# Optimization experiments

Hardware: AMD Instinct MI355X
Metric: run time of the kernel (lower is better)

The kernel has to match this reference:

```python
import jax, jax.numpy as jnp
import numpy as np

NUM_HEADS = 8
BN_EPS = 1e-5


def setup_inputs() -> dict:
    key = jax.random.key(0)
    ks = jax.random.split(key, 8)
    B, Ct, Cs, H, W, E = 8, 256, 128, 32, 32, 256
    s = 0.05  # small init scale to keep softmax logits reasonable
    return {
        "tgt": jax.random.normal(ks[0], (B, Ct, H, W), jnp.float32),
        "src": jax.random.normal(ks[1], (B, Cs, H, W), jnp.float32),
        "kv_w": jax.random.normal(ks[2], (E, Cs), jnp.float32) * s,
        "in_proj_w": jax.random.normal(ks[3], (3 * E, E), jnp.float32) * s,
        "in_proj_b": jnp.zeros((3 * E,), jnp.float32),
        "out_proj_w": jax.random.normal(ks[4], (E, E), jnp.float32) * s,
        "out_proj_b": jnp.zeros((E,), jnp.float32),
        "fuse_w": jax.random.normal(ks[5], (Ct, E), jnp.float32) * s,
        "bn_gamma": jnp.ones((Ct,), jnp.float32),
        "bn_beta": jnp.zeros((Ct,), jnp.float32),
        "bn_mean": jnp.zeros((Ct,), jnp.float32),
        "bn_var": jnp.ones((Ct,), jnp.float32),
    }


def reference(tgt, src, kv_w, in_proj_w, in_proj_b, out_proj_w, out_proj_b,
              fuse_w, bn_gamma, bn_beta, bn_mean, bn_var):
    B, Ct, H, W = tgt.shape
    E = kv_w.shape[0]
    nH = NUM_HEADS
    hd = E // nH

    # q_proj is Identity (C_tgt == embed_dim); flatten spatial to tokens [B, Q, E]
    q_seq = tgt.reshape(B, Ct, H * W).transpose(0, 2, 1)
    # kv_proj: 1x1 conv == channel matmul; then flatten to [B, K, E]
    kv_map = jnp.einsum('bchw,ec->behw', src, kv_w)
    k_seq = kv_map.reshape(B, E, H * W).transpose(0, 2, 1)

    # nn.MultiheadAttention: packed in-projection
    Wq, Wk, Wv = in_proj_w[:E], in_proj_w[E:2 * E], in_proj_w[2 * E:]
    bq, bk, bv = in_proj_b[:E], in_proj_b[E:2 * E], in_proj_b[2 * E:]
    qp = (q_seq @ Wq.T + bq).reshape(B, -1, nH, hd).transpose(0, 2, 1, 3)  # [B,h,Q,d]
    kp = (k_seq @ Wk.T + bk).reshape(B, -1, nH, hd).transpose(0, 2, 1, 3)  # [B,h,K,d]
    vp = (k_seq @ Wv.T + bv).reshape(B, -1, nH, hd).transpose(0, 2, 1, 3)  # [B,h,K,d]

    scores = jnp.einsum('bhqd,bhkd->bhqk', qp, kp) / jnp.sqrt(jnp.float32(hd))
    attn = jax.nn.softmax(scores, axis=-1)  # [B,h,Q,K] (non-flash explicit path)

    ctx = jnp.einsum('bhqk,bhkd->bhqd', attn, vp)
    ctx = ctx.transpose(0, 2, 1, 3).reshape(B, -1, E)  # [B,Q,E]
    out_seq = ctx @ out_proj_w.T + out_proj_b

    # cached spatial key-attention map: mean over heads and queries -> [B,1,Hk,Wk]
    attn_map = attn.mean(axis=(1, 2)).reshape(B, 1, H, W)

    # back to map, fuse: 1x1 conv -> BN(eval) -> SiLU, then residual add
    out_map = out_seq.transpose(0, 2, 1).reshape(B, E, H, W)
    fused = jnp.einsum('behw,ce->bchw', out_map, fuse_w)
    inv = bn_gamma / jnp.sqrt(bn_var + BN_EPS)
    bn = (fused - bn_mean[None, :, None, None]) * inv[None, :, None, None] \
         + bn_beta[None, :, None, None]
    y = tgt + bn * jax.nn.sigmoid(bn)  # SiLU
    return y, attn_map
```

## Files before the change

kernel.cpp:

```cpp
#include <hip/hip_runtime.h>
#include <hip/hip_bf16.h>

typedef unsigned short u16;
typedef __attribute__((ext_vector_type(8))) short short8;
typedef __attribute__((ext_vector_type(4))) float f32x4;
typedef __attribute__((ext_vector_type(4))) unsigned short u16x4;

static __device__ __forceinline__ u16 f2bf(float x) {
  __hip_bfloat16 b = __float2bfloat16(x);
  return *reinterpret_cast<u16*>(&b);
}

#define QSCALE 0.17677669529663687f

__global__ __launch_bounds__(256) void prep_kernel(
    const float* __restrict__ in_proj_w, const float* __restrict__ in_proj_b,
    const float* __restrict__ kv_w, const float* __restrict__ fuse_w,
    const float* __restrict__ out_proj_w, const float* __restrict__ out_proj_b,
    const float* __restrict__ gamma, const float* __restrict__ beta,
    const float* __restrict__ mean, const float* __restrict__ var,
    u16* __restrict__ WqB, u16* __restrict__ WkvB, u16* __restrict__ M2B,
    float* __restrict__ qbias, float2* __restrict__ bnpk) {
  int idx = blockIdx.x * 256 + threadIdx.x;
  if (idx < 65536) {
    WqB[idx] = f2bf(in_proj_w[idx] * QSCALE);
  } else if (idx < 131072) {
    int i = idx - 65536;
    int m = i >> 7, c = i & 127;
    const float* wrow = in_proj_w + (size_t)(256 + m) * 256;
    float s = 0.f;
    for (int e2 = 0; e2 < 256; ++e2) s += wrow[e2] * kv_w[e2 * 128 + c];
    WkvB[i] = f2bf(s);
  } else if (idx < 196608) {
    int i = idx - 131072;
    int c = i >> 8, e2 = i & 255;
    float s = 0.f;
    for (int e = 0; e < 256; ++e)
      s += fuse_w[c * 256 + e] * out_proj_w[e * 256 + e2];
    M2B[i] = f2bf(s);
  } else if (idx < 196864) {
    int c = idx - 196608;
    float fbv = 0.f;
    for (int e = 0; e < 256; ++e) fbv += fuse_w[c * 256 + e] * out_proj_b[e];
    float inv = gamma[c] * rsqrtf(var[c] + 1e-5f);
    bnpk[c] = make_float2(inv, (fbv - mean[c]) * inv + beta[c]);
    qbias[c] = in_proj_b[c] * QSCALE;
  }
}

__global__ __launch_bounds__(256, 3) void qkv_gemm(
    const float* __restrict__ tgt, const float* __restrict__ src,
    const u16* __restrict__ WqB, const u16* __restrict__ WkvB,
    const float* __restrict__ qbias, const float* __restrict__ bkv,
    u16* __restrict__ QB, u16* __restrict__ KB, u16* __restrict__ VB) {
  __shared__ __align__(16) u16 Wl[64 * 40];
  __shared__ __align__(16) u16 Xl[128 * 40];
  int b = blockIdx.z, by = blockIdx.y, n0 = blockIdx.x * 128;
  bool isQ = by < 4;
  int m0 = isQ ? by * 64 : (by - 4) * 64;
  int Kd = isQ ? 256 : 128;
  const u16* Wp = isQ ? WqB : WkvB;
  const float* Xp = isQ ? tgt + (size_t)b * 256 * 1024
                        : src + (size_t)b * 128 * 1024;
  int t = threadIdx.x, wave = t >> 6, lane = t & 63;
  int lq = lane & 15, quad = lane >> 4;
  f32x4 acc[4][2];
#pragma unroll
  for (int mt = 0; mt < 4; ++mt)
#pragma unroll
    for (int nt = 0; nt < 2; ++nt) acc[mt][nt] = (f32x4){0.f, 0.f, 0.f, 0.f};

  for (int k0 = 0; k0 < Kd; k0 += 32) {
    __syncthreads();
    {
      int row = t >> 2, seg = t & 3;
      *(short8*)&Wl[row * 40 + seg * 8] =
          *(const short8*)&Wp[(size_t)(m0 + row) * Kd + k0 + seg * 8];
    }
    for (int i = t; i < 4096; i += 256) {
      int k = i >> 7, n = i & 127;
      Xl[n * 40 + k] = f2bf(Xp[(size_t)(k0 + k) * 1024 + n0 + n]);
    }
    __syncthreads();
    short8 af[4], bf[2];
#pragma unroll
    for (int mt = 0; mt < 4; ++mt)
      af[mt] = *(const short8*)&Wl[(mt * 16 + lq) * 40 + quad * 8];
#pragma unroll
    for (int nt = 0; nt < 2; ++nt)
      bf[nt] = *(const short8*)&Xl[(wave * 32 + nt * 16 + lq) * 40 + quad * 8];
#pragma unroll
    for (int mt = 0; mt < 4; ++mt)
#pragma unroll
      for (int nt = 0; nt < 2; ++nt)
        acc[mt][nt] = __builtin_amdgcn_mfma_f32_16x16x32_bf16(af[mt], bf[nt],
                                                              acc[mt][nt], 0, 0, 0);
  }
  if (isQ) {
#pragma unroll
    for (int mt = 0; mt < 4; ++mt) {
      int e = m0 + mt * 16 + quad * 4;
      f32x4 bi = *(const f32x4*)&qbias[e];
#pragma unroll
      for (int nt = 0; nt < 2; ++nt) {
        int n = n0 + wave * 32 + nt * 16 + lq;
        u16x4 pk;
#pragma unroll
        for (int r = 0; r < 4; ++r) pk[r] = f2bf(acc[mt][nt][r] + bi[r]);
        *(u16x4*)&QB[((size_t)b * 1024 + n) * 256 + e] = pk;
      }
    }
  } else {
#pragma unroll
    for (int mt = 0; mt < 4; ++mt) {
      int m = m0 + mt * 16 + quad * 4;
      f32x4 bi = *(const f32x4*)&bkv[m];
#pragma unroll
      for (int nt = 0; nt < 2; ++nt) {
        int n = n0 + wave * 32 + nt * 16 + lq;
        if (m < 256) {
          int hh = m >> 5, d = m & 31;
          u16x4 pk;
#pragma unroll
          for (int r = 0; r < 4; ++r) pk[r] = f2bf(acc[mt][nt][r] + bi[r]);
          *(u16x4*)&KB[((size_t)(b * 8 + hh) * 1024 + n) * 32 + d] = pk;
        } else {
          int e = m - 256;
#pragma unroll
          for (int r = 0; r < 4; ++r)
            VB[((size_t)b * 256 + e + r) * 1024 + n] = f2bf(acc[mt][nt][r] + bi[r]);
        }
      }
    }
  }
}

__global__ __launch_bounds__(256, 4) void attn_mfma(
    const u16* __restrict__ QB, const u16* __restrict__ KB,
    const u16* __restrict__ VB, u16* __restrict__ ctxB,
    float* __restrict__ attn_out) {
  __shared__ __align__(16) u16 Klds[128 * 40];
  __shared__ __align__(16) u16 Vlds[32 * 136];
  __shared__ __align__(16) u16 Plds[4][32 * 40];
  __shared__ float colsum[1024];

  int b = blockIdx.z, h = blockIdx.y, q0 = blockIdx.x * 128;
  int t = threadIdx.x, wave = t >> 6, lane = t & 63;
  int lq = lane & 15, quad = lane >> 4;

  const u16* Qb = QB + (size_t)b * 1024 * 256 + h * 32;
  const u16* Kb = KB + (size_t)(b * 8 + h) * 1024 * 32;
  const u16* Vb = VB + (size_t)(b * 256 + h * 32) * 1024;

  short8 qf[2];
#pragma unroll
  for (int mt = 0; mt < 2; ++mt)
    qf[mt] = *(const short8*)(Qb + (size_t)(q0 + wave * 32 + mt * 16 + lq) * 256 + quad * 8);

  for (int i = t; i < 1024; i += 256) colsum[i] = 0.f;

  float lsum[2][4];
  f32x4 O[2][2];
#pragma unroll
  for (int mt = 0; mt < 2; ++mt) {
#pragma unroll
    for (int r = 0; r < 4; ++r) lsum[mt][r] = 0.f;
#pragma unroll
    for (int nt = 0; nt < 2; ++nt) O[mt][nt] = (f32x4){0.f, 0.f, 0.f, 0.f};
  }
  const f32x4 zf = (f32x4){0.f, 0.f, 0.f, 0.f};
  u16* Pw = &Plds[wave][0];

  for (int c0 = 0; c0 < 1024; c0 += 128) {
    __syncthreads();
    for (int i = t; i < 512; i += 256)
      *(short8*)&Klds[(i >> 2) * 40 + (i & 3) * 8] =
          *(const short8*)(Kb + (size_t)c0 * 32 + i * 8);
    for (int i = t; i < 512; i += 256) {
      int d = i >> 4, part = i & 15;
      *(short8*)&Vlds[d * 136 + part * 8] =
          *(const short8*)(Vb + (size_t)d * 1024 + c0 + part * 8);
    }
    __syncthreads();
#pragma unroll
    for (int pair = 0; pair < 4; ++pair) {
#pragma unroll
      for (int ntp = 0; ntp < 2; ++ntp) {
        int nt = pair * 2 + ntp;
        short8 kf = *(const short8*)&Klds[(nt * 16 + lq) * 40 + quad * 8];
#pragma unroll
        for (int mt = 0; mt < 2; ++mt) {
          f32x4 s = __builtin_amdgcn_mfma_f32_16x16x32_bf16(qf[mt], kf, zf, 0, 0, 0);
#pragma unroll
          for (int r = 0; r < 4; ++r) {
            float e = __expf(s[r]);
            lsum[mt][r] += e;
            Pw[(mt * 16 + quad * 4 + r) * 40 + ntp * 16 + lq] = f2bf(e);
          }
        }
      }
      short8 pf[2], vf[2];
#pragma unroll
      for (int mt = 0; mt < 2; ++mt)
        pf[mt] = *(const short8*)&Pw[(mt * 16 + lq) * 40 + quad * 8];
#pragma unroll
      for (int nt = 0; nt < 2; ++nt)
        vf[nt] = *(const short8*)&Vlds[(nt * 16 + lq) * 136 + pair * 32 + quad * 8];
#pragma unroll
      for (int mt = 0; mt < 2; ++mt)
#pragma unroll
        for (int nt = 0; nt < 2; ++nt)
          O[mt][nt] = __builtin_amdgcn_mfma_f32_16x16x32_bf16(pf[mt], vf[nt],
                                                              O[mt][nt], 0, 0, 0);
    }
  }

  float linv[2][4];
#pragma unroll
  for (int mt = 0; mt < 2; ++mt)
#pragma unroll
    for (int r = 0; r < 4; ++r) {
      float v = lsum[mt][r];
      v += __shfl_xor(v, 1);
      v += __shfl_xor(v, 2);
      v += __shfl_xor(v, 4);
      v += __shfl_xor(v, 8);
      linv[mt][r] = 1.f / v;
    }

#pragma unroll
  for (int mt = 0; mt < 2; ++mt)
#pragma unroll
    for (int nt = 0; nt < 2; ++nt)
#pragma unroll
      for (int r = 0; r < 4; ++r) {
        int q = q0 + wave * 32 + mt * 16 + quad * 4 + r;
        ctxB[((size_t)b * 1024 + q) * 256 + h * 32 + nt * 16 + lq] =
            f2bf(O[mt][nt][r] * linv[mt][r]);
      }

  for (int c0 = 0; c0 < 1024; c0 += 128) {
    __syncthreads();
    for (int i = t; i < 512; i += 256)
      *(short8*)&Klds[(i >> 2) * 40 + (i & 3) * 8] =
          *(const short8*)(Kb + (size_t)c0 * 32 + i * 8);
    __syncthreads();
#pragma unroll
    for (int nt = 0; nt < 8; ++nt) {
      short8 kf = *(const short8*)&Klds[(nt * 16 + lq) * 40 + quad * 8];
      float cs = 0.f;
#pragma unroll
      for (int mt = 0; mt < 2; ++mt) {
        f32x4 s = __builtin_amdgcn_mfma_f32_16x16x32_bf16(qf[mt], kf, zf, 0, 0, 0);
#pragma unroll
        for (int r = 0; r < 4; ++r) cs += __expf(s[r]) * linv[mt][r];
      }
      cs += __shfl_xor(cs, 16);
      cs += __shfl_xor(cs, 32);
      if (quad == 0) atomicAdd(&colsum[c0 + nt * 16 + lq], cs);
    }
  }
  __syncthreads();
  for (int i = t; i < 1024; i += 256)
    atomicAdd(&attn_out[b * 1024 + i], colsum[i] * (1.f / 8192.f));
}

__global__ __launch_bounds__(256, 3) void fused_out(
    const u16* __restrict__ M2B, const u16* __restrict__ ctxB,
    const float* __restrict__ tgt, const float2* __restrict__ bnpk,
    float* __restrict__ y) {
  __shared__ __align__(16) u16 Al[64 * 40];
  __shared__ __align__(16) u16 Bl[128 * 40];
  int b = blockIdx.z, c0 = blockIdx.y * 64, s0 = blockIdx.x * 128;
  int t = threadIdx.x, wave = t >> 6, lane = t & 63;
  int lq = lane & 15, quad = lane >> 4;
  f32x4 acc[4][2];
#pragma unroll
  for (int mt = 0; mt < 4; ++mt)
#pragma unroll
    for (int nt = 0; nt < 2; ++nt) acc[mt][nt] = (f32x4){0.f, 0.f, 0.f, 0.f};

  for (int k0 = 0; k0 < 256; k0 += 32) {
    __syncthreads();
    {
      int row = t >> 2, seg = t & 3;
      *(short8*)&Al[row * 40 + seg * 8] =
          *(const short8*)&M2B[(size_t)(c0 + row) * 256 + k0 + seg * 8];
    }
    for (int i = t; i < 512; i += 256) {
      int row = i >> 2, seg = i & 3;
      *(short8*)&Bl[row * 40 + seg * 8] =
          *(const short8*)&ctxB[((size_t)b * 1024 + s0 + row) * 256 + k0 + seg * 8];
    }
    __syncthreads();
    short8 af[4], bf[2];
#pragma unroll
    for (int mt = 0; mt < 4; ++mt)
      af[mt] = *(const short8*)&Al[(mt * 16 + lq) * 40 + quad * 8];
#pragma unroll
    for (int nt = 0; nt < 2; ++nt)
      bf[nt] = *(const short8*)&Bl[(wave * 32 + nt * 16 + lq) * 40 + quad * 8];
#pragma unroll
    for (int mt = 0; mt < 4; ++mt)
#pragma unroll
      for (int nt = 0; nt < 2; ++nt)
        acc[mt][nt] = __builtin_amdgcn_mfma_f32_16x16x32_bf16(af[mt], bf[nt],
                                                              acc[mt][nt], 0, 0, 0);
  }
#pragma unroll
  for (int mt = 0; mt < 4; ++mt) {
#pragma unroll
    for (int r = 0; r < 4; ++r) {
      int c = c0 + mt * 16 + quad * 4 + r;
      float2 p = bnpk[c];
#pragma unroll
      for (int nt = 0; nt < 2; ++nt) {
        int s = s0 + wave * 32 + nt * 16 + lq;
        float bn = acc[mt][nt][r] * p.x + p.y;
        float sig = 1.f / (1.f + __expf(-bn));
        size_t idx = ((size_t)b * 256 + c) * 1024 + s;
        y[idx] = tgt[idx] + bn * sig;
      }
    }
  }
}

extern "C" void kernel_launch(void* const* d_in, const int* in_sizes, int n_in,
                              void* d_out, int out_size, void* d_ws, size_t ws_size,
                              hipStream_t stream) {
  const float* tgt = (const float*)d_in[0];
  const float* src = (const float*)d_in[1];
  const float* kv_w = (const float*)d_in[2];
  const float* in_proj_w = (const float*)d_in[3];
  const float* in_proj_b = (const float*)d_in[4];
  const float* out_proj_w = (const float*)d_in[5];
  const float* out_proj_b = (const float*)d_in[6];
  const float* fuse_w = (const float*)d_in[7];
  const float* bn_gamma = (const float*)d_in[8];
  const float* bn_beta = (const float*)d_in[9];
  const float* bn_mean = (const float*)d_in[10];
  const float* bn_var = (const float*)d_in[11];

  char* W = (char*)d_ws;
  u16* WqB = (u16*)W;
  u16* WkvB = (u16*)(W + 131072);
  u16* M2B = (u16*)(W + 262144);
  float* qbias = (float*)(W + 393216);
  float2* bnpk = (float2*)(W + 394240);
  u16* QB = (u16*)(W + 397312);
  u16* KB = QB + 2097152;
  u16* VB = KB + 2097152;
  u16* ctxB = VB + 2097152;

  float* y = (float*)d_out;
  float* attn_out = y + 2097152;

  hipMemsetAsync(attn_out, 0, 8192 * sizeof(float), stream);
  prep_kernel<<<769, 256, 0, stream>>>(in_proj_w, in_proj_b, kv_w, fuse_w,
                                       out_proj_w, out_proj_b, bn_gamma, bn_beta,
                                       bn_mean, bn_var, WqB, WkvB, M2B, qbias, bnpk);
  qkv_gemm<<<dim3(8, 12, 8), 256, 0, stream>>>(tgt, src, WqB, WkvB, qbias,
                                               in_proj_b + 256, QB, KB, VB);
  attn_mfma<<<dim3(8, 8, 8), 256, 0, stream>>>(QB, KB, VB, ctxB, attn_out);
  fused_out<<<dim3(8, 4, 8), 256, 0, stream>>>(M2B, ctxB, tgt, bnpk, y);
}
```

Baseline: 176.9 us.

## Pre-transpose inputs, drop LDS staging in GEMMs, halve attention query tile

Adds a separate transpose kernel that converts tgt/src to token-major bf16, so the QKV GEMM and the output GEMM can load MFMA fragments straight from global memory without LDS staging or barriers. The attention kernel now handles 64 queries per block instead of 128, which doubles the grid, and it writes P with truncating bf16 conversion. The output GEMM also drops to one 16-column tile per wave with a doubled grid. The trade-offs are an extra kernel launch and an extra pass over the input memory, more global loads without reuse, and, in attention, K/V reloaded for twice as many blocks plus slightly less accurate probabilities.

```diff
diff --git a/kernel.cpp b/kernel.cpp
--- a/kernel.cpp
+++ b/kernel.cpp
@@ -9,6 +9,11 @@
 static __device__ __forceinline__ u16 f2bf(float x) {
   __hip_bfloat16 b = __float2bfloat16(x);
   return *reinterpret_cast<u16*>(&b);
+}
+static __device__ __forceinline__ u16 f2bf_trunc(float x) {
+  union { float f; unsigned u; } v;
+  v.f = x;
+  return (u16)(v.u >> 16);
 }
 
 #define QSCALE 0.17677669529663687f
@@ -48,47 +53,67 @@
   }
 }
 
-__global__ __launch_bounds__(256, 3) void qkv_gemm(
+__global__ __launch_bounds__(256) void xpose(
     const float* __restrict__ tgt, const float* __restrict__ src,
+    u16* __restrict__ tgtT, u16* __restrict__ srcT) {
+  __shared__ u16 tile[64 * 65];
+  int b = blockIdx.z, by = blockIdx.y, sb = blockIdx.x * 64;
+  const float* X;
+  u16* XT;
+  int C, cb;
+  if (by < 4) {
+    X = tgt + (size_t)b * 256 * 1024;
+    XT = tgtT + (size_t)b * 1024 * 256;
+    C = 256;
+    cb = by * 64;
+  } else {
+    X = src + (size_t)b * 128 * 1024;
+    XT = srcT + (size_t)b * 1024 * 128;
+    C = 128;
+    cb = (by - 4) * 64;
+  }
+  int t = threadIdx.x;
+  for (int i = t; i < 4096; i += 256) {
+    int c = i >> 6, s = i & 63;
+    tile[c * 65 + s] = f2bf(X[(size_t)(cb + c) * 1024 + sb + s]);
+  }
+  __syncthreads();
+  for (int i = t; i < 4096; i += 256) {
+    int s = i >> 6, c = i & 63;
+    XT[(size_t)(sb + s) * C + cb + c] = tile[c * 65 + s];
+  }
+}
+
+__global__ __launch_bounds__(256) void qkv_gemm(
+    const u16* __restrict__ tgtT, const u16* __restrict__ srcT,
     const u16* __restrict__ WqB, const u16* __restrict__ WkvB,
     const float* __restrict__ qbias, const float* __restrict__ bkv,
     u16* __restrict__ QB, u16* __restrict__ KB, u16* __restrict__ VB) {
-  __shared__ __align__(16) u16 Wl[64 * 40];
-  __shared__ __align__(16) u16 Xl[128 * 40];
-  int b = blockIdx.z, by = blockIdx.y, n0 = blockIdx.x * 128;
-  bool isQ = by < 4;
-  int m0 = isQ ? by * 64 : (by - 4) * 64;
+  int b = blockIdx.z, my = blockIdx.y, n0 = blockIdx.x * 128;
+  bool isQ = my < 4;
+  int m0 = isQ ? my * 64 : (my - 4) * 64;
   int Kd = isQ ? 256 : 128;
   const u16* Wp = isQ ? WqB : WkvB;
-  const float* Xp = isQ ? tgt + (size_t)b * 256 * 1024
-                        : src + (size_t)b * 128 * 1024;
+  const u16* Xp = isQ ? tgtT + (size_t)b * 1024 * 256
+                      : srcT + (size_t)b * 1024 * 128;
   int t = threadIdx.x, wave = t >> 6, lane = t & 63;
   int lq = lane & 15, quad = lane >> 4;
+  int nw = n0 + wave * 32;
   f32x4 acc[4][2];
 #pragma unroll
   for (int mt = 0; mt < 4; ++mt)
 #pragma unroll
     for (int nt = 0; nt < 2; ++nt) acc[mt][nt] = (f32x4){0.f, 0.f, 0.f, 0.f};
 
+#pragma unroll 2
   for (int k0 = 0; k0 < Kd; k0 += 32) {
-    __syncthreads();
-    {
-      int row = t >> 2, seg = t & 3;
-      *(short8*)&Wl[row * 40 + seg * 8] =
-          *(const short8*)&Wp[(size_t)(m0 + row) * Kd + k0 + seg * 8];
-    }
-    for (int i = t; i < 4096; i += 256) {
-      int k = i >> 7, n = i & 127;
-      Xl[n * 40 + k] = f2bf(Xp[(size_t)(k0 + k) * 1024 + n0 + n]);
-    }
-    __syncthreads();
     short8 af[4], bf[2];
 #pragma unroll
     for (int mt = 0; mt < 4; ++mt)
-      af[mt] = *(const short8*)&Wl[(mt * 16 + lq) * 40 + quad * 8];
+      af[mt] = *(const short8*)&Wp[(size_t)(m0 + mt * 16 + lq) * Kd + k0 + quad * 8];
 #pragma unroll
     for (int nt = 0; nt < 2; ++nt)
-      bf[nt] = *(const short8*)&Xl[(wave * 32 + nt * 16 + lq) * 40 + quad * 8];
+      bf[nt] = *(const short8*)&Xp[(size_t)(nw + nt * 16 + lq) * Kd + k0 + quad * 8];
 #pragma unroll
     for (int mt = 0; mt < 4; ++mt)
 #pragma unroll
@@ -103,7 +128,7 @@
       f32x4 bi = *(const f32x4*)&qbias[e];
 #pragma unroll
       for (int nt = 0; nt < 2; ++nt) {
-        int n = n0 + wave * 32 + nt * 16 + lq;
+        int n = nw + nt * 16 + lq;
         u16x4 pk;
 #pragma unroll
         for (int r = 0; r < 4; ++r) pk[r] = f2bf(acc[mt][nt][r] + bi[r]);
@@ -117,7 +142,7 @@
       f32x4 bi = *(const f32x4*)&bkv[m];
 #pragma unroll
       for (int nt = 0; nt < 2; ++nt) {
-        int n = n0 + wave * 32 + nt * 16 + lq;
+        int n = nw + nt * 16 + lq;
         if (m < 256) {
           int hh = m >> 5, d = m & 31;
           u16x4 pk;
@@ -135,16 +160,16 @@
   }
 }
 
-__global__ __launch_bounds__(256, 4) void attn_mfma(
+__global__ __launch_bounds__(256) void attn_mfma(
     const u16* __restrict__ QB, const u16* __restrict__ KB,
     const u16* __restrict__ VB, u16* __restrict__ ctxB,
     float* __restrict__ attn_out) {
   __shared__ __align__(16) u16 Klds[128 * 40];
   __shared__ __align__(16) u16 Vlds[32 * 136];
-  __shared__ __align__(16) u16 Plds[4][32 * 40];
+  __shared__ __align__(16) u16 Plds[4][16 * 48];
   __shared__ float colsum[1024];
 
-  int b = blockIdx.z, h = blockIdx.y, q0 = blockIdx.x * 128;
+  int b = blockIdx.z, h = blockIdx.y, q0 = blockIdx.x * 64;
   int t = threadIdx.x, wave = t >> 6, lane = t & 63;
   int lq = lane & 15, quad = lane >> 4;
 
@@ -152,22 +177,12 @@
   const u16* Kb = KB + (size_t)(b * 8 + h) * 1024 * 32;
   const u16* Vb = VB + (size_t)(b * 256 + h * 32) * 1024;
 
-  short8 qf[2];
-#pragma unroll
-  for (int mt = 0; mt < 2; ++mt)
-    qf[mt] = *(const short8*)(Qb + (size_t)(q0 + wave * 32 + mt * 16 + lq) * 256 + quad * 8);
+  short8 qf = *(const short8*)(Qb + (size_t)(q0 + wave * 16 + lq) * 256 + quad * 8);
 
   for (int i = t; i < 1024; i += 256) colsum[i] = 0.f;
 
-  float lsum[2][4];
-  f32x4 O[2][2];
-#pragma unroll
-  for (int mt = 0; mt < 2; ++mt) {
-#pragma unroll
-    for (int r = 0; r < 4; ++r) lsum[mt][r] = 0.f;
-#pragma unroll
-    for (int nt = 0; nt < 2; ++nt) O[mt][nt] = (f32x4){0.f, 0.f, 0.f, 0.f};
-  }
+  float lsum[4] = {0.f, 0.f, 0.f, 0.f};
+  f32x4 O[2] = {(f32x4){0.f, 0.f, 0.f, 0.f}, (f32x4){0.f, 0.f, 0.f, 0.f}};
   const f32x4 zf = (f32x4){0.f, 0.f, 0.f, 0.f};
   u16* Pw = &Plds[wave][0];
 
@@ -188,56 +203,41 @@
       for (int ntp = 0; ntp < 2; ++ntp) {
         int nt = pair * 2 + ntp;
         short8 kf = *(const short8*)&Klds[(nt * 16 + lq) * 40 + quad * 8];
-#pragma unroll
-        for (int mt = 0; mt < 2; ++mt) {
-          f32x4 s = __builtin_amdgcn_mfma_f32_16x16x32_bf16(qf[mt], kf, zf, 0, 0, 0);
-#pragma unroll
-          for (int r = 0; r < 4; ++r) {
-            float e = __expf(s[r]);
-            lsum[mt][r] += e;
-            Pw[(mt * 16 + quad * 4 + r) * 40 + ntp * 16 + lq] = f2bf(e);
-          }
+        f32x4 s = __builtin_amdgcn_mfma_f32_16x16x32_bf16(qf, kf, zf, 0, 0, 0);
+#pragma unroll
+        for (int r = 0; r < 4; ++r) {
+          float e = __expf(s[r]);
+          lsum[r] += e;
+          Pw[(quad * 4 + r) * 48 + ntp * 16 + lq] = f2bf_trunc(e);
         }
       }
-      short8 pf[2], vf[2];
-#pragma unroll
-      for (int mt = 0; mt < 2; ++mt)
-        pf[mt] = *(const short8*)&Pw[(mt * 16 + lq) * 40 + quad * 8];
-#pragma unroll
-      for (int nt = 0; nt < 2; ++nt)
-        vf[nt] = *(const short8*)&Vlds[(nt * 16 + lq) * 136 + pair * 32 + quad * 8];
-#pragma unroll
-      for (int mt = 0; mt < 2; ++mt)
-#pragma unroll
-        for (int nt = 0; nt < 2; ++nt)
-          O[mt][nt] = __builtin_amdgcn_mfma_f32_16x16x32_bf16(pf[mt], vf[nt],
-                                                              O[mt][nt], 0, 0, 0);
-    }
-  }
-
-  float linv[2][4];
-#pragma unroll
-  for (int mt = 0; mt < 2; ++mt)
+      short8 pf = *(const short8*)&Pw[lq * 48 + quad * 8];
+      short8 vf0 = *(const short8*)&Vlds[(0 * 16 + lq) * 136 + pair * 32 + quad * 8];
+      short8 vf1 = *(const short8*)&Vlds[(1 * 16 + lq) * 136 + pair * 32 + quad * 8];
+      O[0] = __builtin_amdgcn_mfma_f32_16x16x32_bf16(pf, vf0, O[0], 0, 0, 0);
+      O[1] = __builtin_amdgcn_mfma_f32_16x16x32_bf16(pf, vf1, O[1], 0, 0, 0);
+    }
+  }
+
+  float linv[4];
+#pragma unroll
+  for (int r = 0; r < 4; ++r) {
+    float v = lsum[r];
+    v += __shfl_xor(v, 1);
+    v += __shfl_xor(v, 2);
+    v += __shfl_xor(v, 4);
+    v += __shfl_xor(v, 8);
+    linv[r] = 1.f / v;
+  }
+
+#pragma unroll
+  for (int nt = 0; nt < 2; ++nt)
 #pragma unroll
     for (int r = 0; r < 4; ++r) {
-      float v = lsum[mt][r];
-      v += __shfl_xor(v, 1);
-      v += __shfl_xor(v, 2);
-      v += __shfl_xor(v, 4);
-      v += __shfl_xor(v, 8);
-      linv[mt][r] = 1.f / v;
-    }
-
-#pragma unroll
-  for (int mt = 0; mt < 2; ++mt)
-#pragma unroll
-    for (int nt = 0; nt < 2; ++nt)
-#pragma unroll
-      for (int r = 0; r < 4; ++r) {
-        int q = q0 + wave * 32 + mt * 16 + quad * 4 + r;
-        ctxB[((size_t)b * 1024 + q) * 256 + h * 32 + nt * 16 + lq] =
-            f2bf(O[mt][nt][r] * linv[mt][r]);
-      }
+      int q = q0 + wave * 16 + quad * 4 + r;
+      ctxB[((size_t)b * 1024 + q) * 256 + h * 32 + nt * 16 + lq] =
+          f2bf(O[nt][r] * linv[r]);
+    }
 
   for (int c0 = 0; c0 < 1024; c0 += 128) {
     __syncthreads();
@@ -248,13 +248,10 @@
 #pragma unroll
     for (int nt = 0; nt < 8; ++nt) {
       short8 kf = *(const short8*)&Klds[(nt * 16 + lq) * 40 + quad * 8];
+      f32x4 s = __builtin_amdgcn_mfma_f32_16x16x32_bf16(qf, kf, zf, 0, 0, 0);
       float cs = 0.f;
 #pragma unroll
-      for (int mt = 0; mt < 2; ++mt) {
-        f32x4 s = __builtin_amdgcn_mfma_f32_16x16x32_bf16(qf[mt], kf, zf, 0, 0, 0);
-#pragma unroll
-        for (int r = 0; r < 4; ++r) cs += __expf(s[r]) * linv[mt][r];
-      }
+      for (int r = 0; r < 4; ++r) cs += __expf(s[r]) * linv[r];
       cs += __shfl_xor(cs, 16);
       cs += __shfl_xor(cs, 32);
       if (quad == 0) atomicAdd(&colsum[c0 + nt * 16 + lq], cs);
@@ -265,62 +262,40 @@
     atomicAdd(&attn_out[b * 1024 + i], colsum[i] * (1.f / 8192.f));
 }
 
-__global__ __launch_bounds__(256, 3) void fused_out(
+__global__ __launch_bounds__(256) void fused_out(
     const u16* __restrict__ M2B, const u16* __restrict__ ctxB,
     const float* __restrict__ tgt, const float2* __restrict__ bnpk,
     float* __restrict__ y) {
-  __shared__ __align__(16) u16 Al[64 * 40];
-  __shared__ __align__(16) u16 Bl[128 * 40];
-  int b = blockIdx.z, c0 = blockIdx.y * 64, s0 = blockIdx.x * 128;
+  int b = blockIdx.z, c0 = blockIdx.y * 64;
   int t = threadIdx.x, wave = t >> 6, lane = t & 63;
   int lq = lane & 15, quad = lane >> 4;
-  f32x4 acc[4][2];
-#pragma unroll
-  for (int mt = 0; mt < 4; ++mt)
-#pragma unroll
-    for (int nt = 0; nt < 2; ++nt) acc[mt][nt] = (f32x4){0.f, 0.f, 0.f, 0.f};
-
+  int s0 = blockIdx.x * 64 + wave * 16;
+  f32x4 acc[4];
+#pragma unroll
+  for (int mt = 0; mt < 4; ++mt) acc[mt] = (f32x4){0.f, 0.f, 0.f, 0.f};
+
+#pragma unroll 4
   for (int k0 = 0; k0 < 256; k0 += 32) {
-    __syncthreads();
-    {
-      int row = t >> 2, seg = t & 3;
-      *(short8*)&Al[row * 40 + seg * 8] =
-          *(const short8*)&M2B[(size_t)(c0 + row) * 256 + k0 + seg * 8];
-    }
-    for (int i = t; i < 512; i += 256) {
-      int row = i >> 2, seg = i & 3;
-      *(short8*)&Bl[row * 40 + seg * 8] =
-          *(const short8*)&ctxB[((size_t)b * 1024 + s0 + row) * 256 + k0 + seg * 8];
-    }
-    __syncthreads();
-    short8 af[4], bf[2];
+    short8 bf = *(const short8*)&ctxB[((size_t)b * 1024 + s0 + lq) * 256 + k0 + quad * 8];
+    short8 af[4];
 #pragma unroll
     for (int mt = 0; mt < 4; ++mt)
-      af[mt] = *(const short8*)&Al[(mt * 16 + lq) * 40 + quad * 8];
-#pragma unroll
-    for (int nt = 0; nt < 2; ++nt)
-      bf[nt] = *(const short8*)&Bl[(wave * 32 + nt * 16 + lq) * 40 + quad * 8];
+      af[mt] = *(const short8*)&M2B[(size_t)(c0 + mt * 16 + lq) * 256 + k0 + quad * 8];
 #pragma unroll
     for (int mt = 0; mt < 4; ++mt)
-#pragma unroll
-      for (int nt = 0; nt < 2; ++nt)
-        acc[mt][nt] = __builtin_amdgcn_mfma_f32_16x16x32_bf16(af[mt], bf[nt],
-                                                              acc[mt][nt], 0, 0, 0);
-  }
+      acc[mt] = __builtin_amdgcn_mfma_f32_16x16x32_bf16(af[mt], bf, acc[mt], 0, 0, 0);
+  }
+  int s = s0 + lq;
 #pragma unroll
   for (int mt = 0; mt < 4; ++mt) {
 #pragma unroll
     for (int r = 0; r < 4; ++r) {
       int c = c0 + mt * 16 + quad * 4 + r;
       float2 p = bnpk[c];
-#pragma unroll
-      for (int nt = 0; nt < 2; ++nt) {
-        int s = s0 + wave * 32 + nt * 16 + lq;
-        float bn = acc[mt][nt][r] * p.x + p.y;
-        float sig = 1.f / (1.f + __expf(-bn));
-        size_t idx = ((size_t)b * 256 + c) * 1024 + s;
-        y[idx] = tgt[idx] + bn * sig;
-      }
+      float bn = acc[mt][r] * p.x + p.y;
+      float sig = 1.f / (1.f + __expf(-bn));
+      size_t idx = ((size_t)b * 256 + c) * 1024 + s;
+      y[idx] = tgt[idx] + bn * sig;
     }
   }
 }
@@ -347,7 +322,9 @@
   u16* M2B = (u16*)(W + 262144);
   float* qbias = (float*)(W + 393216);
   float2* bnpk = (float2*)(W + 394240);
-  u16* QB = (u16*)(W + 397312);
+  u16* tgtT = (u16*)(W + 397312);
+  u16* srcT = tgtT + 2097152;
+  u16* QB = srcT + 1048576;
   u16* KB = QB + 2097152;
   u16* VB = KB + 2097152;
   u16* ctxB = VB + 2097152;
@@ -359,8 +336,9 @@
   prep_kernel<<<769, 256, 0, stream>>>(in_proj_w, in_proj_b, kv_w, fuse_w,
                                        out_proj_w, out_proj_b, bn_gamma, bn_beta,
                                        bn_mean, bn_var, WqB, WkvB, M2B, qbias, bnpk);
-  qkv_gemm<<<dim3(8, 12, 8), 256, 0, stream>>>(tgt, src, WqB, WkvB, qbias,
+  xpose<<<dim3(16, 6, 8), 256, 0, stream>>>(tgt, src, tgtT, srcT);
+  qkv_gemm<<<dim3(8, 12, 8), 256, 0, stream>>>(tgtT, srcT, WqB, WkvB, qbias,
                                                in_proj_b + 256, QB, KB, VB);
-  attn_mfma<<<dim3(8, 8, 8), 256, 0, stream>>>(QB, KB, VB, ctxB, attn_out);
-  fused_out<<<dim3(8, 4, 8), 256, 0, stream>>>(M2B, ctxB, tgt, bnpk, y);
-}
+  attn_mfma<<<dim3(16, 8, 8), 256, 0, stream>>>(QB, KB, VB, ctxB, attn_out);
+  fused_out<<<dim3(16, 4, 8), 256, 0, stream>>>(M2B, ctxB, tgt, bnpk, y);
+}
```

Result: slower. 194.6 us (+10.0%).
